# Kernel tuning notes

Measured on AMD Instinct MI355X. Metric: run time of the kernel, lower is better.

The kernel has to match this reference:

```python
import jax, jax.numpy as jnp
import numpy as np

N_ATOMS = 100000   # real atoms (index 0 is padding row -> total rows N_ATOMS+1)
N_BONDS = 200000   # real directed bonds (index 0 is padding row)
MAX_NB = 6
HIDDEN = 300
ATOM_FDIM = 133
BOND_FDIM = 147
DEPTH = 3
N_MOLS = 5000
ATOMS_PER_MOL = N_ATOMS // N_MOLS


def setup_inputs() -> dict:
    key = jax.random.key(0)
    ks = jax.random.split(key, 8)
    f_atoms = jax.random.normal(ks[0], (N_ATOMS + 1, ATOM_FDIM), dtype=jnp.float32)
    f_atoms = f_atoms.at[0].set(0.0)  # chemprop zero-padding row
    f_bonds = jax.random.normal(ks[1], (N_BONDS + 1, BOND_FDIM), dtype=jnp.float32)
    f_bonds = f_bonds.at[0].set(0.0)
    # weights (Linear stored as [in, out]); bias=False for W_i/W_h, W_o has bias
    W_i = jax.random.normal(ks[2], (BOND_FDIM, HIDDEN), dtype=jnp.float32) * 0.05
    W_h = jax.random.normal(ks[3], (HIDDEN, HIDDEN), dtype=jnp.float32) * 0.05
    W_o = jax.random.normal(ks[4], (ATOM_FDIM + HIDDEN, HIDDEN), dtype=jnp.float32) * 0.05
    b_o = jnp.zeros((HIDDEN,), dtype=jnp.float32)
    # a2b: incoming bond ids per atom, padded with 0 (padding row of message is 0)
    a2b = jax.random.randint(ks[5], (N_ATOMS + 1, MAX_NB), 0, N_BONDS + 1, dtype=jnp.int32)
    a2b = a2b.at[0].set(0)
    # b2a: source atom of each bond
    b2a = jax.random.randint(ks[6], (N_BONDS + 1,), 1, N_ATOMS + 1, dtype=jnp.int32)
    b2a = b2a.at[0].set(0)
    # b2revb: reverse-bond pairing; bonds (2k+1, 2k+2) are partners, 0 -> 0
    idx = jnp.arange(N_BONDS + 1, dtype=jnp.int32)
    b2revb = jnp.where(idx == 0, 0, ((idx - 1) ^ 1) + 1).astype(jnp.int32)
    # molecule segment id for each real atom (replaces a_scope loop)
    mol_ids = (jnp.arange(N_ATOMS, dtype=jnp.int32) // ATOMS_PER_MOL).astype(jnp.int32)
    return {"f_atoms": f_atoms, "f_bonds": f_bonds, "W_i": W_i, "W_h": W_h,
            "W_o": W_o, "b_o": b_o, "a2b": a2b, "b2a": b2a, "b2revb": b2revb,
            "mol_ids": mol_ids}


def reference(f_atoms, f_bonds, W_i, W_h, W_o, b_o, a2b, b2a, b2revb, mol_ids):
    # input = act(W_i(f_bonds))  (ReLU, bias=False)
    inp = jax.nn.relu(f_bonds @ W_i)                    # [B+1, H]
    message = inp
    for _ in range(DEPTH - 1):
        nei = message[a2b]                              # [A+1, MAX_NB, H] gather
        a_message = nei.sum(axis=1)                     # [A+1, H]
        message = a_message[b2a] - message[b2revb]      # [B+1, H]
        message = jax.nn.relu(inp + message @ W_h)      # skip-connection + act
    # final atom readout
    a_message = message[a2b].sum(axis=1)                # [A+1, H]
    a_input = jnp.concatenate([f_atoms, a_message], axis=1)
    atom_hiddens = jax.nn.relu(a_input @ W_o + b_o)     # [A+1, H]
    # per-molecule mean pooling over real atoms (rows 1:)
    real = atom_hiddens[1:]                             # [A, H]
    sums = jax.ops.segment_sum(real, mol_ids, num_segments=N_MOLS)
    counts = jax.ops.segment_sum(jnp.ones((N_ATOMS,), dtype=real.dtype), mol_ids,
                                 num_segments=N_MOLS)
    mol_vecs = sums / jnp.maximum(counts, 1.0)[:, None]  # [N_MOLS, H]
    return mol_vecs
```

## Files before the change

kernel.cpp:

```cpp
#include <hip/hip_runtime.h>
#include <hip/hip_bf16.h>

#define N_ATOMS   100000
#define N_BONDS   200000
#define MAX_NB    6
#define HIDDEN    300
#define ATOM_FDIM 133
#define BOND_FDIM 147
#define N_MOLS    5000
#define APM       20

#define MB_ROWS (N_BONDS + 1)
#define MA_ROWS (N_ATOMS + 1)

#define CHUNKS_B 1280
#define EPS      308
#define ROWP     65

typedef unsigned short bf16_t;
typedef __attribute__((ext_vector_type(8))) __bf16 bf16x8;
typedef __attribute__((ext_vector_type(4))) float  float4v;

__device__ __forceinline__ float bf2f(unsigned short u) {
    union { unsigned int i; float f; } x; x.i = ((unsigned int)u) << 16; return x.f;
}
__device__ __forceinline__ unsigned short f2bf(float f) {
    union { float f; unsigned int i; } x; x.f = f;
    unsigned int r = x.i + 0x7FFFu + ((x.i >> 16) & 1u);
    return (unsigned short)(r >> 16);
}

__global__ __launch_bounds__(256) void prep_w(
    const float* __restrict__ W, bf16_t* __restrict__ dst, int K,
    int total_chunks, int perm)
{
    int idx = blockIdx.x * 256 + threadIdx.x;
    if (idx >= total_chunks) return;
    int kb  = idx / CHUNKS_B;
    int c   = idx - kb * CHUNKS_B;
    int cq  = c / 320;
    int col = c - cq * 320;
    unsigned short v[8];
    #pragma unroll
    for (int j = 0; j < 8; ++j) {
        int k = kb * 32 + cq * 8 + j;
        int ksrc;
        if (perm) ksrc = (k < 133) ? k : ((k >= 136 && k < 436) ? k - 3 : -1);
        else      ksrc = (k < K) ? k : -1;
        float f = (ksrc >= 0 && col < HIDDEN) ? W[(size_t)ksrc * HIDDEN + col] : 0.f;
        v[j] = f2bf(f);
    }
    bf16_t* p = dst + (size_t)idx * 8;
    *(ushort4*)(p)     = make_ushort4(v[0], v[1], v[2], v[3]);
    *(ushort4*)(p + 4) = make_ushort4(v[4], v[5], v[6], v[7]);
}

template<int MODE, int KB>
__global__ __launch_bounds__(512, 4) void gemm_mfma(
    const float* __restrict__ Af,
    const bf16_t* __restrict__ Ab1, const bf16_t* __restrict__ Ab2,
    const int* __restrict__ b2a, const int* __restrict__ b2revb,
    const bf16_t* __restrict__ WB, const float* __restrict__ bias,
    const bf16_t* __restrict__ addend, bf16_t* __restrict__ Y,
    int M)
{
    const int S = HIDDEN;
    constexpr int QG = KB * 4;
    constexpr int NT = (64 * QG + 511) / 512;
    constexpr int ASZ = QG * ROWP * 16;
    constexpr int LDS_BYTES = (ASZ > 16 * EPS * 4) ? ASZ : 16 * EPS * 4;
    __shared__ __align__(16) char lds_pool[LDS_BYTES];
    bf16_t* As  = (bf16_t*)lds_pool;
    float*  epi = (float*)lds_pool;
    __shared__ int rowmap[128];

    const int tid  = threadIdx.x;
    const int lane = tid & 63;
    const int w    = tid >> 6;
    const int wm   = w >> 2;
    const int wn   = w & 3;
    const int lrow = lane & 15;
    const int q    = lane >> 4;
    const int bm   = blockIdx.x * 64;

    if (MODE == 1) {
        if (tid < 64) {
            int sr = bm + tid;
            rowmap[tid] = (sr < M) ? b2a[sr] : 0;
        } else if (tid < 128) {
            int sr = bm + tid - 64;
            rowmap[tid] = (sr < M) ? b2revb[sr] : 0;
        }
        __syncthreads();
    }

    ushort4 A0[NT], A1[NT], C0[NT], C1[NT];
    float   F[(MODE == 1) ? 1 : NT][8];
    const ushort4 zz = make_ushort4(0, 0, 0, 0);

    #pragma unroll
    for (int i = 0; i < NT; ++i) {
        int t = tid + i * 512;
        if (t < 64 * QG) {
            int row = t / QG;
            int qg  = t - row * QG;
            int k0  = qg * 8;
            if (MODE == 1) {
                const bf16_t* pa = Ab1 + (size_t)rowmap[row]      * S;
                const bf16_t* pc = Ab2 + (size_t)rowmap[64 + row] * S;
                A0[i] = (k0 + 4 <= S) ? *(const ushort4*)(pa + k0)     : zz;
                A1[i] = (k0 + 8 <= S) ? *(const ushort4*)(pa + k0 + 4) : zz;
                C0[i] = (k0 + 4 <= S) ? *(const ushort4*)(pc + k0)     : zz;
                C1[i] = (k0 + 8 <= S) ? *(const ushort4*)(pc + k0 + 4) : zz;
            } else if (MODE == 0) {
                int srow = bm + row;
                #pragma unroll
                for (int j = 0; j < 8; ++j) {
                    int k = k0 + j;
                    F[i][j] = (srow < M && k < BOND_FDIM)
                              ? Af[(size_t)srow * BOND_FDIM + k] : 0.f;
                }
            } else {
                int srow = bm + row;
                if (k0 < 136) {
                    #pragma unroll
                    for (int j = 0; j < 8; ++j) {
                        int k = k0 + j;
                        F[i][j] = (srow < M && k < ATOM_FDIM)
                                  ? Af[(size_t)srow * ATOM_FDIM + k] : 0.f;
                    }
                } else {
                    int off = k0 - 136;
                    const bf16_t* pm = Ab1 + (size_t)srow * S;
                    ushort4 u0 = (srow < M && off + 4 <= S)
                                 ? *(const ushort4*)(pm + off)     : zz;
                    ushort4 u1 = (srow < M && off + 8 <= S)
                                 ? *(const ushort4*)(pm + off + 4) : zz;
                    *(ushort4*)&F[i][0] = u0;
                    *(ushort4*)&F[i][2] = u1;
                }
            }
        }
    }

    #pragma unroll
    for (int i = 0; i < NT; ++i) {
        int t = tid + i * 512;
        if (t < 64 * QG) {
            int row = t / QG;
            int qg  = t - row * QG;
            unsigned short av[8];
            if (MODE == 1) {
                av[0] = f2bf(bf2f(A0[i].x) - bf2f(C0[i].x));
                av[1] = f2bf(bf2f(A0[i].y) - bf2f(C0[i].y));
                av[2] = f2bf(bf2f(A0[i].z) - bf2f(C0[i].z));
                av[3] = f2bf(bf2f(A0[i].w) - bf2f(C0[i].w));
                av[4] = f2bf(bf2f(A1[i].x) - bf2f(C1[i].x));
                av[5] = f2bf(bf2f(A1[i].y) - bf2f(C1[i].y));
                av[6] = f2bf(bf2f(A1[i].z) - bf2f(C1[i].z));
                av[7] = f2bf(bf2f(A1[i].w) - bf2f(C1[i].w));
            } else if (MODE == 0) {
                #pragma unroll
                for (int j = 0; j < 8; ++j) av[j] = f2bf(F[i][j]);
            } else {
                int k0 = qg * 8;
                if (k0 < 136) {
                    #pragma unroll
                    for (int j = 0; j < 8; ++j) av[j] = f2bf(F[i][j]);
                } else {
                    ushort4 u0 = *(const ushort4*)&F[i][0];
                    ushort4 u1 = *(const ushort4*)&F[i][2];
                    av[0] = u0.x; av[1] = u0.y; av[2] = u0.z; av[3] = u0.w;
                    av[4] = u1.x; av[5] = u1.y; av[6] = u1.z; av[7] = u1.w;
                }
            }
            bf16_t* dst = As + (size_t)(qg * ROWP + row) * 8;
            *(ushort4*)(dst)     = make_ushort4(av[0], av[1], av[2], av[3]);
            *(ushort4*)(dst + 4) = make_ushort4(av[4], av[5], av[6], av[7]);
        }
    }

    float4v acc[2][5];
    #pragma unroll
    for (int i = 0; i < 2; ++i)
        #pragma unroll
        for (int j = 0; j < 5; ++j) {
            float4v z = {0.f, 0.f, 0.f, 0.f};
            acc[i][j] = z;
        }

    __syncthreads();

    const bf16_t* wptr = WB + (size_t)(q * 320 + wn * 80 + lrow) * 8;
    bf16x8 bcur[5], bnxt[5];
    #pragma unroll
    for (int nt = 0; nt < 5; ++nt)
        bcur[nt] = *(const bf16x8*)(wptr + nt * 128);

    #pragma unroll
    for (int kb = 0; kb < KB; ++kb) {
        const bf16_t* abase = As + (size_t)((kb * 4 + q) * ROWP + wm * 32 + lrow) * 8;
        bf16x8 af0 = *(const bf16x8*)(abase);
        bf16x8 af1 = *(const bf16x8*)(abase + 16 * 8);
        if (kb + 1 < KB) {
            const bf16_t* wnx = wptr + (size_t)(kb + 1) * (CHUNKS_B * 8);
            #pragma unroll
            for (int nt = 0; nt < 5; ++nt)
                bnxt[nt] = *(const bf16x8*)(wnx + nt * 128);
        }
        #pragma unroll
        for (int nt = 0; nt < 5; ++nt) {
            if (wn * 80 + nt * 16 < HIDDEN) {
                acc[0][nt] = __builtin_amdgcn_mfma_f32_16x16x32_bf16(af0, bcur[nt], acc[0][nt], 0, 0, 0);
                acc[1][nt] = __builtin_amdgcn_mfma_f32_16x16x32_bf16(af1, bcur[nt], acc[1][nt], 0, 0, 0);
            }
        }
        if (kb + 1 < KB) {
            #pragma unroll
            for (int nt = 0; nt < 5; ++nt) bcur[nt] = bnxt[nt];
        }
    }

    __syncthreads();
    #pragma unroll
    for (int mt = 0; mt < 2; ++mt) {
        for (int wh = 0; wh < 2; ++wh) {
            if (wm == wh) {
                #pragma unroll
                for (int nt = 0; nt < 5; ++nt) {
                    const int c0 = wn * 80 + nt * 16;
                    if (c0 < HIDDEN) {
                        #pragma unroll
                        for (int r = 0; r < 4; ++r)
                            epi[(q * 4 + r) * EPS + c0 + lrow] = acc[mt][nt][r];
                    }
                }
            }
            __syncthreads();
            const int row0 = bm + wh * 32 + mt * 16;
            for (int s = tid; s < 16 * 75; s += 512) {
                int rr = s / 75;
                int c4 = s - rr * 75;
                int grow = row0 + rr;
                if (grow < M) {
                    float4 v = *(const float4*)&epi[rr * EPS + c4 * 4];
                    if (MODE == 1) {
                        ushort4 ad = *(const ushort4*)(addend + (size_t)grow * S + c4 * 4);
                        v.x += bf2f(ad.x); v.y += bf2f(ad.y);
                        v.z += bf2f(ad.z); v.w += bf2f(ad.w);
                    }
                    if (MODE == 2) {
                        float4 bv = *(const float4*)(bias + c4 * 4);
                        v.x += bv.x; v.y += bv.y; v.z += bv.z; v.w += bv.w;
                    }
                    ushort4 o;
                    o.x = f2bf(v.x > 0.f ? v.x : 0.f);
                    o.y = f2bf(v.y > 0.f ? v.y : 0.f);
                    o.z = f2bf(v.z > 0.f ? v.z : 0.f);
                    o.w = f2bf(v.w > 0.f ? v.w : 0.f);
                    *(ushort4*)(Y + (size_t)grow * S + c4 * 4) = o;
                }
            }
            __syncthreads();
        }
    }
}

__global__ __launch_bounds__(256) void aggregate_k(
    const bf16_t* __restrict__ msg, const int* __restrict__ a2b,
    bf16_t* __restrict__ amsg)
{
    int idx = blockIdx.x * blockDim.x + threadIdx.x;
    const int total = MA_ROWS * 25;
    if (idx >= total) return;
    int a  = idx / 25;
    int g  = idx - a * 25;
    int c0 = g * 12;
    const int* nb = a2b + (size_t)a * MAX_NB;
    int b[MAX_NB];
    #pragma unroll
    for (int j = 0; j < MAX_NB; ++j) b[j] = nb[j];
    ushort4 u0[MAX_NB], u1[MAX_NB], u2[MAX_NB];
    #pragma unroll
    for (int j = 0; j < MAX_NB; ++j) {
        const bf16_t* p = msg + (size_t)b[j] * HIDDEN + c0;
        u0[j] = *(const ushort4*)(p);
        u1[j] = *(const ushort4*)(p + 4);
        u2[j] = *(const ushort4*)(p + 8);
    }
    float s[12];
    #pragma unroll
    for (int k = 0; k < 12; ++k) s[k] = 0.f;
    #pragma unroll
    for (int j = 0; j < MAX_NB; ++j) {
        s[0] += bf2f(u0[j].x); s[1]  += bf2f(u0[j].y);
        s[2] += bf2f(u0[j].z); s[3]  += bf2f(u0[j].w);
        s[4] += bf2f(u1[j].x); s[5]  += bf2f(u1[j].y);
        s[6] += bf2f(u1[j].z); s[7]  += bf2f(u1[j].w);
        s[8] += bf2f(u2[j].x); s[9]  += bf2f(u2[j].y);
        s[10]+= bf2f(u2[j].z); s[11] += bf2f(u2[j].w);
    }
    bf16_t* o = amsg + (size_t)a * HIDDEN + c0;
    *(ushort4*)(o)     = make_ushort4(f2bf(s[0]), f2bf(s[1]), f2bf(s[2]),  f2bf(s[3]));
    *(ushort4*)(o + 4) = make_ushort4(f2bf(s[4]), f2bf(s[5]), f2bf(s[6]),  f2bf(s[7]));
    *(ushort4*)(o + 8) = make_ushort4(f2bf(s[8]), f2bf(s[9]), f2bf(s[10]), f2bf(s[11]));
}

__global__ __launch_bounds__(256) void mol_mean_k(
    const bf16_t* __restrict__ atom_h, float* __restrict__ out)
{
    int idx = blockIdx.x * blockDim.x + threadIdx.x;
    if (idx >= N_MOLS * 75) return;
    int m  = idx / 75;
    int c4 = idx - m * 75;
    const bf16_t* base = atom_h + (size_t)(1 + m * APM) * HIDDEN + c4 * 4;
    float4 s = make_float4(0.f, 0.f, 0.f, 0.f);
    #pragma unroll
    for (int i = 0; i < APM; ++i) {
        ushort4 u = *(const ushort4*)(base + (size_t)i * HIDDEN);
        s.x += bf2f(u.x); s.y += bf2f(u.y); s.z += bf2f(u.z); s.w += bf2f(u.w);
    }
    const float inv = 1.0f / (float)APM;
    s.x *= inv; s.y *= inv; s.z *= inv; s.w *= inv;
    *(float4*)(out + (size_t)m * HIDDEN + c4 * 4) = s;
}

extern "C" void kernel_launch(void* const* d_in, const int* in_sizes, int n_in,
                              void* d_out, int out_size, void* d_ws, size_t ws_size,
                              hipStream_t stream)
{
    const float* f_atoms = (const float*)d_in[0];
    const float* f_bonds = (const float*)d_in[1];
    const float* W_i     = (const float*)d_in[2];
    const float* W_h     = (const float*)d_in[3];
    const float* W_o     = (const float*)d_in[4];
    const float* b_o     = (const float*)d_in[5];
    const int*   a2b     = (const int*)d_in[6];
    const int*   b2a     = (const int*)d_in[7];
    const int*   b2revb  = (const int*)d_in[8];
    float* out = (float*)d_out;

    char* base = (char*)d_ws;
    const size_t SZ_BOND_B = (((size_t)MB_ROWS * HIDDEN * sizeof(bf16_t)) + 255) & ~(size_t)255;
    bf16_t* inp  = (bf16_t*)(base);
    bf16_t* msgA = (bf16_t*)(base + SZ_BOND_B);
    bf16_t* amsg = (bf16_t*)(base + 2 * SZ_BOND_B);

    char* scratch = (char*)d_out;
    bf16_t* Wib = (bf16_t*)(scratch);
    bf16_t* Whb = (bf16_t*)(scratch + 102400);
    bf16_t* Wob = (bf16_t*)(scratch + 307200);

    dim3 blk512(512), blk256(256);
    const int gb = (MB_ROWS + 63) / 64;
    const int ga = (MA_ROWS + 63) / 64;
    int agg_blocks  = (MA_ROWS * 25 + 255) / 256;
    int mean_blocks = (N_MOLS * 75 + 255) / 256;

    prep_w<<<(5  * CHUNKS_B + 255) / 256, blk256, 0, stream>>>(W_i, Wib, BOND_FDIM, 5 * CHUNKS_B, 0);
    prep_w<<<(10 * CHUNKS_B + 255) / 256, blk256, 0, stream>>>(W_h, Whb, HIDDEN, 10 * CHUNKS_B, 0);
    prep_w<<<(14 * CHUNKS_B + 255) / 256, blk256, 0, stream>>>(W_o, Wob, 436, 14 * CHUNKS_B, 1);

    gemm_mfma<0, 5><<<gb, blk512, 0, stream>>>(
        f_bonds, nullptr, nullptr, nullptr, nullptr,
        Wib, nullptr, nullptr, inp, MB_ROWS);

    aggregate_k<<<agg_blocks, blk256, 0, stream>>>(inp, a2b, amsg);
    gemm_mfma<1, 10><<<gb, blk512, 0, stream>>>(
        nullptr, amsg, inp, b2a, b2revb,
        Whb, nullptr, inp, msgA, MB_ROWS);

    aggregate_k<<<agg_blocks, blk256, 0, stream>>>(msgA, a2b, amsg);
    gemm_mfma<1, 10><<<gb, blk512, 0, stream>>>(
        nullptr, amsg, msgA, b2a, b2revb,
        Whb, nullptr, inp, inp, MB_ROWS);

    aggregate_k<<<agg_blocks, blk256, 0, stream>>>(inp, a2b, amsg);
    gemm_mfma<2, 14><<<ga, blk512, 0, stream>>>(
        f_atoms, amsg, nullptr, nullptr, nullptr,
        Wob, b_o, nullptr, msgA, MA_ROWS);

    mol_mean_k<<<mean_blocks, blk256, 0, stream>>>(msgA, out);
}
```

Baseline: 849.4 us.

## Make GEMM staging loads branchless, hoist weight prefetch, and double per-thread aggregation work

The GEMM prologue now builds predicated addresses first and then issues all gathered loads unconditionally. Out-of-range lanes read a valid dummy address, so the loads are no longer behind branches and can stay in flight together. The first weight-fragment load is moved ahead of the LDS staging so it overlaps with it. The aggregation kernel now handles two atom/column tasks per thread, which doubles the loads in flight per thread but raises register pressure and halves the grid.

```diff
diff --git a/kernel.cpp b/kernel.cpp
--- a/kernel.cpp
+++ b/kernel.cpp
@@ -65,9 +65,10 @@
     int M)
 {
     const int S = HIDDEN;
-    constexpr int QG = KB * 4;
-    constexpr int NT = (64 * QG + 511) / 512;
-    constexpr int ASZ = QG * ROWP * 16;
+    constexpr int QG    = KB * 4;
+    constexpr int TASKS = 64 * QG;
+    constexpr int NT    = (TASKS + 511) / 512;
+    constexpr int ASZ   = QG * ROWP * 16;
     constexpr int LDS_BYTES = (ASZ > 16 * EPS * 4) ? ASZ : 16 * EPS * 4;
     __shared__ __align__(16) char lds_pool[LDS_BYTES];
     bf16_t* As  = (bf16_t*)lds_pool;
@@ -94,59 +95,85 @@
         __syncthreads();
     }
 
+    #define ACT(i) ((TASKS % 512 == 0) || (((i) + 1) * 512 <= TASKS) || (tid + (i) * 512 < TASKS))
+
     ushort4 A0[NT], A1[NT], C0[NT], C1[NT];
     float   F[(MODE == 1) ? 1 : NT][8];
-    const ushort4 zz = make_ushort4(0, 0, 0, 0);
-
-    #pragma unroll
-    for (int i = 0; i < NT; ++i) {
-        int t = tid + i * 512;
-        if (t < 64 * QG) {
+
+    if (MODE == 1) {
+        const bf16_t* gA0[NT]; const bf16_t* gA1[NT];
+        const bf16_t* gC0[NT]; const bf16_t* gC1[NT];
+        #pragma unroll
+        for (int i = 0; i < NT; ++i) {
+            int t   = tid + i * 512;
             int row = t / QG;
             int qg  = t - row * QG;
             int k0  = qg * 8;
-            if (MODE == 1) {
-                const bf16_t* pa = Ab1 + (size_t)rowmap[row]      * S;
-                const bf16_t* pc = Ab2 + (size_t)rowmap[64 + row] * S;
-                A0[i] = (k0 + 4 <= S) ? *(const ushort4*)(pa + k0)     : zz;
-                A1[i] = (k0 + 8 <= S) ? *(const ushort4*)(pa + k0 + 4) : zz;
-                C0[i] = (k0 + 4 <= S) ? *(const ushort4*)(pc + k0)     : zz;
-                C1[i] = (k0 + 8 <= S) ? *(const ushort4*)(pc + k0 + 4) : zz;
-            } else if (MODE == 0) {
+            const bf16_t* pa = Ab1 + (size_t)rowmap[row]      * S;
+            const bf16_t* pc = Ab2 + (size_t)rowmap[64 + row] * S;
+            gA0[i] = (k0 + 4 <= S) ? pa + k0     : Ab1;
+            gA1[i] = (k0 + 8 <= S) ? pa + k0 + 4 : Ab1;
+            gC0[i] = (k0 + 4 <= S) ? pc + k0     : Ab1;
+            gC1[i] = (k0 + 8 <= S) ? pc + k0 + 4 : Ab1;
+        }
+        #pragma unroll
+        for (int i = 0; i < NT; ++i) {
+            A0[i] = *(const ushort4*)gA0[i];
+            A1[i] = *(const ushort4*)gA1[i];
+            C0[i] = *(const ushort4*)gC0[i];
+            C1[i] = *(const ushort4*)gC1[i];
+        }
+    } else if (MODE == 0) {
+        #pragma unroll
+        for (int i = 0; i < NT; ++i) {
+            if (ACT(i)) {
+                int t = tid + i * 512;
+                int row = t / QG, qg = t - row * QG, k0 = qg * 8;
                 int srow = bm + row;
+                int base = srow * BOND_FDIM;
                 #pragma unroll
                 for (int j = 0; j < 8; ++j) {
                     int k = k0 + j;
-                    F[i][j] = (srow < M && k < BOND_FDIM)
-                              ? Af[(size_t)srow * BOND_FDIM + k] : 0.f;
+                    F[i][j] = Af[(srow < M && k < BOND_FDIM) ? base + k : 0];
+                }
+            }
+        }
+    } else {
+        #pragma unroll
+        for (int i = 0; i < NT; ++i) {
+            int t = tid + i * 512;
+            int row = t / QG, qg = t - row * QG, k0 = qg * 8;
+            int srow = bm + row;
+            if (k0 < 136) {
+                int base = srow * ATOM_FDIM;
+                #pragma unroll
+                for (int j = 0; j < 8; ++j) {
+                    int k = k0 + j;
+                    F[i][j] = Af[(srow < M && k < ATOM_FDIM) ? base + k : 0];
                 }
             } else {
-                int srow = bm + row;
-                if (k0 < 136) {
-                    #pragma unroll
-                    for (int j = 0; j < 8; ++j) {
-                        int k = k0 + j;
-                        F[i][j] = (srow < M && k < ATOM_FDIM)
-                                  ? Af[(size_t)srow * ATOM_FDIM + k] : 0.f;
-                    }
-                } else {
-                    int off = k0 - 136;
-                    const bf16_t* pm = Ab1 + (size_t)srow * S;
-                    ushort4 u0 = (srow < M && off + 4 <= S)
-                                 ? *(const ushort4*)(pm + off)     : zz;
-                    ushort4 u1 = (srow < M && off + 8 <= S)
-                                 ? *(const ushort4*)(pm + off + 4) : zz;
-                    *(ushort4*)&F[i][0] = u0;
-                    *(ushort4*)&F[i][2] = u1;
-                }
-            }
-        }
-    }
+                int off = k0 - 136;
+                const bf16_t* pm = Ab1 + (size_t)srow * S;
+                const bf16_t* g0 = (srow < M && off + 4 <= S) ? pm + off     : Ab1;
+                const bf16_t* g1 = (srow < M && off + 8 <= S) ? pm + off + 4 : Ab1;
+                ushort4 u0 = *(const ushort4*)g0;
+                ushort4 u1 = *(const ushort4*)g1;
+                *(ushort4*)&F[i][0] = u0;
+                *(ushort4*)&F[i][2] = u1;
+            }
+        }
+    }
+
+    const bf16_t* wptr = WB + (size_t)(q * 320 + wn * 80 + lrow) * 8;
+    bf16x8 bcur[5], bnxt[5];
+    #pragma unroll
+    for (int nt = 0; nt < 5; ++nt)
+        bcur[nt] = *(const bf16x8*)(wptr + nt * 128);
 
     #pragma unroll
     for (int i = 0; i < NT; ++i) {
-        int t = tid + i * 512;
-        if (t < 64 * QG) {
+        if (ACT(i)) {
+            int t = tid + i * 512;
             int row = t / QG;
             int qg  = t - row * QG;
             unsigned short av[8];
@@ -179,6 +206,7 @@
             *(ushort4*)(dst + 4) = make_ushort4(av[4], av[5], av[6], av[7]);
         }
     }
+    #undef ACT
 
     float4v acc[2][5];
     #pragma unroll
@@ -190,12 +218,6 @@
         }
 
     __syncthreads();
-
-    const bf16_t* wptr = WB + (size_t)(q * 320 + wn * 80 + lrow) * 8;
-    bf16x8 bcur[5], bnxt[5];
-    #pragma unroll
-    for (int nt = 0; nt < 5; ++nt)
-        bcur[nt] = *(const bf16x8*)(wptr + nt * 128);
 
     #pragma unroll
     for (int kb = 0; kb < KB; ++kb) {
@@ -266,44 +288,65 @@
     }
 }
 
-__global__ __launch_bounds__(256) void aggregate_k(
+__global__ __launch_bounds__(256, 4) void aggregate_k(
     const bf16_t* __restrict__ msg, const int* __restrict__ a2b,
     bf16_t* __restrict__ amsg)
 {
-    int idx = blockIdx.x * blockDim.x + threadIdx.x;
-    const int total = MA_ROWS * 25;
-    if (idx >= total) return;
-    int a  = idx / 25;
-    int g  = idx - a * 25;
-    int c0 = g * 12;
-    const int* nb = a2b + (size_t)a * MAX_NB;
-    int b[MAX_NB];
-    #pragma unroll
-    for (int j = 0; j < MAX_NB; ++j) b[j] = nb[j];
-    ushort4 u0[MAX_NB], u1[MAX_NB], u2[MAX_NB];
+    constexpr int TOT  = MA_ROWS * 25;
+    constexpr int HALF = (TOT + 1) / 2;
+    int i0 = blockIdx.x * 256 + threadIdx.x;
+    if (i0 >= HALF) return;
+    int  i1   = i0 + HALF;
+    bool has1 = (i1 < TOT);
+    int  i1c  = has1 ? i1 : 0;
+    int a0 = i0 / 25,  g0 = i0 - a0 * 25,  c0 = g0 * 12;
+    int a1 = i1c / 25, g1 = i1c - a1 * 25, c1 = g1 * 12;
+
+    const int* nb0 = a2b + (size_t)a0 * MAX_NB;
+    const int* nb1 = a2b + (size_t)a1 * MAX_NB;
+    int b0[MAX_NB], b1[MAX_NB];
+    #pragma unroll
+    for (int j = 0; j < MAX_NB; ++j) { b0[j] = nb0[j]; b1[j] = nb1[j]; }
+
+    ushort4 u0[MAX_NB][3], u1[MAX_NB][3];
     #pragma unroll
     for (int j = 0; j < MAX_NB; ++j) {
-        const bf16_t* p = msg + (size_t)b[j] * HIDDEN + c0;
-        u0[j] = *(const ushort4*)(p);
-        u1[j] = *(const ushort4*)(p + 4);
-        u2[j] = *(const ushort4*)(p + 8);
-    }
-    float s[12];
-    #pragma unroll
-    for (int k = 0; k < 12; ++k) s[k] = 0.f;
+        const bf16_t* p = msg + (size_t)b0[j] * HIDDEN + c0;
+        u0[j][0] = *(const ushort4*)(p);
+        u0[j][1] = *(const ushort4*)(p + 4);
+        u0[j][2] = *(const ushort4*)(p + 8);
+    }
     #pragma unroll
     for (int j = 0; j < MAX_NB; ++j) {
-        s[0] += bf2f(u0[j].x); s[1]  += bf2f(u0[j].y);
-        s[2] += bf2f(u0[j].z); s[3]  += bf2f(u0[j].w);
-        s[4] += bf2f(u1[j].x); s[5]  += bf2f(u1[j].y);
-        s[6] += bf2f(u1[j].z); s[7]  += bf2f(u1[j].w);
-        s[8] += bf2f(u2[j].x); s[9]  += bf2f(u2[j].y);
-        s[10]+= bf2f(u2[j].z); s[11] += bf2f(u2[j].w);
-    }
-    bf16_t* o = amsg + (size_t)a * HIDDEN + c0;
-    *(ushort4*)(o)     = make_ushort4(f2bf(s[0]), f2bf(s[1]), f2bf(s[2]),  f2bf(s[3]));
-    *(ushort4*)(o + 4) = make_ushort4(f2bf(s[4]), f2bf(s[5]), f2bf(s[6]),  f2bf(s[7]));
-    *(ushort4*)(o + 8) = make_ushort4(f2bf(s[8]), f2bf(s[9]), f2bf(s[10]), f2bf(s[11]));
+        const bf16_t* p = msg + (size_t)b1[j] * HIDDEN + c1;
+        u1[j][0] = *(const ushort4*)(p);
+        u1[j][1] = *(const ushort4*)(p + 4);
+        u1[j][2] = *(const ushort4*)(p + 8);
+    }
+
+    float s0[12], s1[12];
+    #pragma unroll
+    for (int k = 0; k < 12; ++k) { s0[k] = 0.f; s1[k] = 0.f; }
+    #pragma unroll
+    for (int j = 0; j < MAX_NB; ++j) {
+        #pragma unroll
+        for (int h = 0; h < 3; ++h) {
+            s0[h*4+0] += bf2f(u0[j][h].x); s0[h*4+1] += bf2f(u0[j][h].y);
+            s0[h*4+2] += bf2f(u0[j][h].z); s0[h*4+3] += bf2f(u0[j][h].w);
+            s1[h*4+0] += bf2f(u1[j][h].x); s1[h*4+1] += bf2f(u1[j][h].y);
+            s1[h*4+2] += bf2f(u1[j][h].z); s1[h*4+3] += bf2f(u1[j][h].w);
+        }
+    }
+    bf16_t* o0 = amsg + (size_t)a0 * HIDDEN + c0;
+    *(ushort4*)(o0)     = make_ushort4(f2bf(s0[0]), f2bf(s0[1]), f2bf(s0[2]),  f2bf(s0[3]));
+    *(ushort4*)(o0 + 4) = make_ushort4(f2bf(s0[4]), f2bf(s0[5]), f2bf(s0[6]),  f2bf(s0[7]));
+    *(ushort4*)(o0 + 8) = make_ushort4(f2bf(s0[8]), f2bf(s0[9]), f2bf(s0[10]), f2bf(s0[11]));
+    if (has1) {
+        bf16_t* o1 = amsg + (size_t)a1 * HIDDEN + c1;
+        *(ushort4*)(o1)     = make_ushort4(f2bf(s1[0]), f2bf(s1[1]), f2bf(s1[2]),  f2bf(s1[3]));
+        *(ushort4*)(o1 + 4) = make_ushort4(f2bf(s1[4]), f2bf(s1[5]), f2bf(s1[6]),  f2bf(s1[7]));
+        *(ushort4*)(o1 + 8) = make_ushort4(f2bf(s1[8]), f2bf(s1[9]), f2bf(s1[10]), f2bf(s1[11]));
+    }
 }
 
 __global__ __launch_bounds__(256) void mol_mean_k(
@@ -354,7 +397,8 @@
     dim3 blk512(512), blk256(256);
     const int gb = (MB_ROWS + 63) / 64;
     const int ga = (MA_ROWS + 63) / 64;
-    int agg_blocks  = (MA_ROWS * 25 + 255) / 256;
+    const int agg_tasks  = ((MA_ROWS * 25) + 1) / 2;
+    int agg_blocks  = (agg_tasks + 255) / 256;
     int mean_blocks = (N_MOLS * 75 + 255) / 256;
 
     prep_w<<<(5  * CHUNKS_B + 255) / 256, blk256, 0, stream>>>(W_i, Wib, BOND_FDIM, 5 * CHUNKS_B, 0);
```

After: 817.8 us. 1.04x faster.
